# Performance work log

Hardware: AMD Instinct MI355X
Metric: run time of the kernel (lower is better)

Reference implementation:

```python
import jax, jax.numpy as jnp
import numpy as np

EPS = 1e-5

def _rms(x, w):
    v = jnp.mean(jnp.square(x.astype(jnp.float32)), axis=-1, keepdims=True)
    return (x * jax.lax.rsqrt(v + EPS)) * w

def _rope(x, f):
    # x: [B,S,H,hd]; f: [S,1,hd//2,2,2]
    x_ = x.astype(jnp.float32).reshape(*x.shape[:-1], -1, 1, 2)
    out = f[..., 0] * x_[..., 0] + f[..., 1] * x_[..., 1]  # [B,S,H,hd//2,2]
    return out.reshape(x.shape).astype(x.dtype)

def setup_inputs() -> dict:
    key = jax.random.key(0)
    ks = jax.random.split(key, 32)
    B, L, D = 2, 2048, 1024
    ns, enc = 2, 128
    H, hd = 16, 64
    S = enc + L // ns  # 1152 joint seq per stage
    std = 0.02
    w = lambda k, shp: (jax.random.normal(k, shp, jnp.float32) * std)
    inp = {}
    inp['hidden_states'] = jax.random.normal(ks[0], (B, L, D), jnp.float32)
    inp['encoder_hidden_states'] = jax.random.normal(ks[1], (B * ns, enc, D), jnp.float32)
    inp['attention_mask'] = jnp.zeros((ns, B, 1, S, S), jnp.float32)
    inp['image_rotary_emb'] = jax.random.normal(ks[2], (ns, S, 1, hd // 2, 2, 2), jnp.float32)
    names = ['Wq', 'Wk', 'Wv', 'Waq', 'Wak', 'Wav']
    for i, n in enumerate(names):
        inp[n] = w(ks[3 + i], (D, D))
        inp['b' + n[1:]] = jnp.zeros((D,), jnp.float32)
    inp['Wo'] = w(ks[9], (D, D)); inp['bo'] = jnp.zeros((D,), jnp.float32)
    inp['Wao'] = w(ks[10], (D, D)); inp['bao'] = jnp.zeros((D,), jnp.float32)
    for n in ['gq', 'gk', 'gaq', 'gak']:
        inp[n] = jnp.ones((hd,), jnp.float32)
    inp['hidden_length'] = jnp.array([L // ns] * ns, jnp.int32)
    return inp

def reference(hidden_states, encoder_hidden_states, attention_mask, image_rotary_emb,
              Wq, bq, Wk, bk, Wv, bv, Waq, baq, Wak, bak, Wav, bav,
              Wo, bo, Wao, bao, gq, gk, gaq, gak, hidden_length):
    lengths = [int(v) for v in np.asarray(hidden_length)]
    ns = len(lengths)
    B = hidden_states.shape[0]
    enc = encoder_hidden_states.shape[1]
    hd = gq.shape[0]
    H = Wq.shape[0] // hd
    scale = hd ** -0.5
    lin = lambda x, W, b: jnp.einsum('bsd,od->bso', x, W) + b
    proj = lambda x, W, b: lin(x, W, b).reshape(x.shape[0], -1, H, hd)
    q = _rms(proj(hidden_states, Wq, bq), gq)
    k = _rms(proj(hidden_states, Wk, bk), gk)
    v = proj(hidden_states, Wv, bv)
    eq = _rms(proj(encoder_hidden_states, Waq, baq), gaq)
    ek = _rms(proj(encoder_hidden_states, Wak, bak), gak)
    ev = proj(encoder_hidden_states, Wav, bav)
    outs_h, outs_e = [], []
    i_sum = 0
    for i_p, length in enumerate(lengths):
        cq = jnp.concatenate([eq[i_p::ns], q[:, i_sum:i_sum + length]], axis=1)
        ck = jnp.concatenate([ek[i_p::ns], k[:, i_sum:i_sum + length]], axis=1)
        cv = jnp.concatenate([ev[i_p::ns], v[:, i_sum:i_sum + length]], axis=1)
        f = image_rotary_emb[i_p]
        cq = _rope(cq, f)
        ck = _rope(ck, f)
        s = jnp.einsum('bqhd,bkhd->bhqk', cq, ck) * scale + attention_mask[i_p]
        a = jax.nn.softmax(s, axis=-1)
        o = jnp.einsum('bhqk,bkhd->bqhd', a, cv).reshape(B, -1, H * hd)
        outs_e.append(o[:, :enc])
        outs_h.append(o[:, enc:])
        i_sum += length
    enc_out = jnp.stack(outs_e, axis=1).reshape(B * ns, enc, H * hd)
    hid = jnp.concatenate(outs_h, axis=1)
    hid = lin(hid, Wo, bo)
    enc_out = lin(enc_out, Wao, bao)
    return (hid, enc_out)
```

## Files before the change

kernel.cpp:

```cpp
#include <hip/hip_runtime.h>
#include <stdint.h>


typedef unsigned short u16;
typedef unsigned int u32;
typedef short bf16x8 __attribute__((ext_vector_type(8)));
typedef short bf16x4 __attribute__((ext_vector_type(4)));
typedef float f32x4 __attribute__((ext_vector_type(4)));

__device__ __forceinline__ u16 f2bf(float f) {
  union { float f; u32 i; } v; v.f = f;
  u32 u = v.i;
  return (u16)((u + 0x7FFFu + ((u >> 16) & 1u)) >> 16);
}
__device__ __forceinline__ u32 pk2(float a, float b) {
  return (u32)f2bf(a) | ((u32)f2bf(b) << 16);
}

#if __has_builtin(__builtin_amdgcn_mfma_f32_16x16x16_bf16)
#define MFMA16(a, b, c) __builtin_amdgcn_mfma_f32_16x16x16_bf16(a, b, c, 0, 0, 0)
#elif __has_builtin(__builtin_amdgcn_mfma_f32_16x16x16bf16_1k)
#define MFMA16(a, b, c) __builtin_amdgcn_mfma_f32_16x16x16bf16_1k(a, b, c, 0, 0, 0)
#else
__device__ __forceinline__ f32x4 mfma16_asm(bf16x4 a, bf16x4 b, f32x4 c) {
  asm volatile("v_mfma_f32_16x16x16_bf16 %0, %1, %2, %0" : "+v"(c) : "v"(a), "v"(b));
  return c;
}
#define MFMA16(a, b, c) mfma16_asm(a, b, c)
#endif

#define GLD16(g, l)                                                        \
  __builtin_amdgcn_global_load_lds(                                        \
      (const __attribute__((address_space(1))) void*)(uintptr_t)(g),       \
      (__attribute__((address_space(3))) void*)(uintptr_t)(l), 16, 0, 0)

#define WS_QJ 0u
#define WS_KJ 4718592u
#define WS_VT 9437184u
#define WS_OJ 14155776u
#define WS_HS 18874368u
#define WS_EHS 23068672u
#define WS_W0 23592960u

struct ConvArgs {
  const float* src[10];
  u32 dst_off[10];
  u32 blk_prefix[11];
};

__global__ __launch_bounds__(256) void conv_f32_bf16(ConvArgs a, u16* __restrict__ ws) {
  const int b = blockIdx.x;
  int t = 0;
#pragma unroll
  for (int i = 0; i < 9; ++i) t += (b >= (int)a.blk_prefix[i + 1]) ? 1 : 0;
  const int chunk = b - (int)a.blk_prefix[t];
  const int base = chunk * 2048 + threadIdx.x * 8;
  const float4* s = (const float4*)(a.src[t] + base);
  const float4 v0 = s[0];
  const float4 v1 = s[1];
  uint4 o;
  o.x = pk2(v0.x, v0.y); o.y = pk2(v0.z, v0.w);
  o.z = pk2(v1.x, v1.y); o.w = pk2(v1.z, v1.w);
  *(uint4*)(ws + a.dst_off[t] + base) = o;
}

__global__ __launch_bounds__(256) void proj_qkv(
    u16* __restrict__ ws,
    const float* __restrict__ bq, const float* __restrict__ bk, const float* __restrict__ bv,
    const float* __restrict__ baq, const float* __restrict__ bak, const float* __restrict__ bav,
    const float* __restrict__ gq, const float* __restrict__ gk,
    const float* __restrict__ gaq, const float* __restrict__ gak,
    const float* __restrict__ rot) {
  __shared__ __align__(16) char lds[32768];
  const int tid = threadIdx.x;
  const int lane = tid & 63;
  const int w = tid >> 6;
  const int wm = w >> 1, wn = w & 1;
  const int quad = lane >> 4;
  const int l15 = lane & 15;

  const int bx = blockIdx.x;
  const int by = blockIdx.y;
  const int wsel = by >> 3;
  const int nb = by & 7;
  const bool is_enc = (bx >= 32);

  const u16* Asrc = is_enc ? (ws + WS_EHS + (size_t)(bx - 32) * 131072)
                           : (ws + WS_HS + (size_t)bx * 131072);
  const u16* Wsrc = ws + WS_W0 + (size_t)(wsel + (is_enc ? 3 : 0)) * 1048576 +
                    (size_t)nb * 131072;
  const float* bsel;
  const float* gsel = gq;
  if (wsel == 0) { bsel = is_enc ? baq : bq; gsel = is_enc ? gaq : gq; }
  else if (wsel == 1) { bsel = is_enc ? bak : bk; gsel = is_enc ? gak : gk; }
  else { bsel = is_enc ? bav : bv; }

  f32x4 acc[4][4] = {};

  for (int kb = 0; kb < 16; ++kb) {
    __syncthreads();
#pragma unroll
    for (int j = 0; j < 4; ++j) {
      const int sidx = j * 256 + w * 64 + lane;
      const int r = sidx >> 3;
      const int kc = (sidx & 7) ^ (r & 7);
      GLD16(Asrc + (size_t)r * 1024 + kb * 64 + kc * 8, lds + j * 4096 + w * 1024);
      GLD16(Wsrc + (size_t)r * 1024 + kb * 64 + kc * 8, lds + 16384 + j * 4096 + w * 1024);
    }
    __syncthreads();
#pragma unroll
    for (int ks = 0; ks < 2; ++ks) {
      bf16x8 af[4], bw[4];
      const int c = ks * 4 + quad;
#pragma unroll
      for (int t = 0; t < 4; ++t) {
        const int ra = wm * 64 + t * 16 + l15;
        af[t] = *(const bf16x8*)(lds + ra * 128 + ((c ^ (ra & 7)) << 4));
        const int rb = wn * 64 + t * 16 + l15;
        bw[t] = *(const bf16x8*)(lds + 16384 + rb * 128 + ((c ^ (rb & 7)) << 4));
      }
#pragma unroll
      for (int rt = 0; rt < 4; ++rt)
#pragma unroll
        for (int ct = 0; ct < 4; ++ct)
          acc[rt][ct] = __builtin_amdgcn_mfma_f32_16x16x32_bf16(af[rt], bw[ct], acc[rt][ct], 0, 0, 0);
    }
  }

  const int n0 = nb * 128 + wn * 64;
  float biasv[4], gv[4];
#pragma unroll
  for (int ct = 0; ct < 4; ++ct) {
    biasv[ct] = bsel[n0 + ct * 16 + l15];
    gv[ct] = (wsel < 2) ? gsel[ct * 16 + l15] * (wsel == 0 ? 0.125f : 1.0f) : 0.f;
  }

  if (wsel == 2) {
    u16* vt = ws + WS_VT;
#pragma unroll
    for (int rt = 0; rt < 4; ++rt) {
      const int m0 = bx * 128 + wm * 64 + rt * 16 + quad * 4;
      int sb, spos0;
      if (is_enc) {
        const int mp = m0 - 4096;
        const int eb = mp >> 7;
        sb = ((eb & 1) << 1) + (eb >> 1);
        spos0 = mp & 127;
      } else {
        const int b = m0 >> 11;
        const int ip = (m0 >> 10) & 1;
        sb = ip * 2 + b;
        spos0 = 128 + (m0 & 1023);
      }
#pragma unroll
      for (int ct = 0; ct < 4; ++ct) {
        const int d = n0 + ct * 16 + l15;
        uint2 pk;
        pk.x = pk2(acc[rt][ct][0] + biasv[ct], acc[rt][ct][1] + biasv[ct]);
        pk.y = pk2(acc[rt][ct][2] + biasv[ct], acc[rt][ct][3] + biasv[ct]);
        *(uint2*)(vt + (size_t)sb * 1179648 + (size_t)d * 1152 + spos0) = pk;
      }
    }
  } else {
    u16* dst = ws + (wsel == 0 ? WS_QJ : WS_KJ);
#pragma unroll
    for (int rt = 0; rt < 4; ++rt) {
#pragma unroll
      for (int rg = 0; rg < 4; ++rg) {
        const int m = bx * 128 + wm * 64 + rt * 16 + quad * 4 + rg;
        int sb, spos;
        if (is_enc) {
          const int mp = m - 4096;
          const int eb = mp >> 7;
          sb = ((eb & 1) << 1) + (eb >> 1);
          spos = mp & 127;
        } else {
          const int b = m >> 11;
          const int ip = (m >> 10) & 1;
          sb = ip * 2 + b;
          spos = 128 + (m & 1023);
        }
        float vals[4];
#pragma unroll
        for (int ct = 0; ct < 4; ++ct) vals[ct] = acc[rt][ct][rg] + biasv[ct];
        float ssq = vals[0] * vals[0] + vals[1] * vals[1] + vals[2] * vals[2] + vals[3] * vals[3];
        ssq += __shfl_xor(ssq, 1);
        ssq += __shfl_xor(ssq, 2);
        ssq += __shfl_xor(ssq, 4);
        ssq += __shfl_xor(ssq, 8);
        const float sc = rsqrtf(ssq * 0.015625f + 1e-5f);
        const int ip = sb >> 1;
        const float* rf = rot + (size_t)(ip * 1152 + spos) * 128;
#pragma unroll
        for (int ct = 0; ct < 4; ++ct) {
          const float v = vals[ct] * sc * gv[ct];
          const float o = __shfl_xor(v, 1);
          const int d = ct * 16 + l15;
          const float f0 = rf[(d >> 1) * 4 + (d & 1) * 2];
          const float f1 = rf[(d >> 1) * 4 + (d & 1) * 2 + 1];
          vals[ct] = (d & 1) ? (f0 * o + f1 * v) : (f0 * v + f1 * o);
        }
        u16* drow = dst + ((size_t)sb * 1152 + spos) * 1024 + n0;
#pragma unroll
        for (int ct = 0; ct < 4; ++ct) drow[ct * 16 + l15] = f2bf(vals[ct]);
      }
    }
  }
}

__global__ __launch_bounds__(256) void attn(u16* __restrict__ ws) {
  __shared__ __align__(16) char lds[40960];
  const int tid = threadIdx.x;
  const int lane = tid & 63;
  const int w = tid >> 6;
  const int quad = lane >> 4;
  const int l15 = lane & 15;
  const int qb = blockIdx.x;
  const int h = blockIdx.y;
  const int sb = blockIdx.z;

  const u16* Qsrc = ws + WS_QJ + (size_t)sb * 1179648 + h * 64;
  const u16* Ksrc = ws + WS_KJ + (size_t)sb * 1179648 + h * 64;
  const u16* Vsrc = ws + WS_VT + (size_t)sb * 1179648 + (size_t)(h * 64) * 1152;

  char* Qs = lds;
  char* Ks = lds + 8192;
  char* Vt = lds + 24576;

#pragma unroll
  for (int j = 0; j < 2; ++j) {
    const int sidx = j * 256 + w * 64 + lane;
    const int r = sidx >> 3;
    const int kc = (sidx & 7) ^ (r & 7);
    GLD16(Qsrc + (size_t)(qb * 64 + r) * 1024 + kc * 8, Qs + j * 4096 + w * 1024);
  }

  f32x4 oacc[4] = {};
  float m2row = -1e30f, lrow = 0.f;
  const int rqw = w * 16 + l15;
  const float LOG2E = 1.4426950408889634f;

  for (int nc = 0; nc < 9; ++nc) {
    __syncthreads();
#pragma unroll
    for (int j = 0; j < 4; ++j) {
      const int sidx = j * 256 + w * 64 + lane;
      const int r = sidx >> 3;
      const int kc = (sidx & 7) ^ (r & 7);
      GLD16(Ksrc + (size_t)(nc * 128 + r) * 1024 + kc * 8, Ks + j * 4096 + w * 1024);
    }
#pragma unroll
    for (int j = 0; j < 4; ++j) {
      const int sidx = j * 256 + w * 64 + lane;
      const int r = sidx >> 4;
      const int kc = (sidx & 15) ^ (r & 15);
      GLD16(Vsrc + (size_t)r * 1152 + nc * 128 + kc * 8, Vt + j * 4096 + w * 1024);
    }
    __syncthreads();

    f32x4 sacc[8] = {};
#pragma unroll
    for (int ks = 0; ks < 2; ++ks) {
      const int c = ks * 4 + quad;
      const bf16x8 bq = *(const bf16x8*)(Qs + rqw * 128 + ((c ^ (rqw & 7)) << 4));
#pragma unroll
      for (int ct = 0; ct < 8; ++ct) {
        const int rk = ct * 16 + l15;
        const bf16x8 ak = *(const bf16x8*)(Ks + rk * 128 + ((c ^ (rk & 7)) << 4));
        sacc[ct] = __builtin_amdgcn_mfma_f32_16x16x32_bf16(ak, bq, sacc[ct], 0, 0, 0);
      }
    }

    float mx = -1e30f;
#pragma unroll
    for (int ct = 0; ct < 8; ++ct) {
#pragma unroll
      for (int rg = 0; rg < 4; ++rg) {
        sacc[ct][rg] *= LOG2E;
        mx = fmaxf(mx, sacc[ct][rg]);
      }
    }
    mx = fmaxf(mx, __shfl_xor(mx, 16));
    mx = fmaxf(mx, __shfl_xor(mx, 32));
    const float m2new = fmaxf(m2row, mx);
    const float alpha = exp2f(m2row - m2new);
    m2row = m2new;
    float sum = 0.f;
#pragma unroll
    for (int ct = 0; ct < 8; ++ct) {
#pragma unroll
      for (int rg = 0; rg < 4; ++rg) {
        const float p = exp2f(sacc[ct][rg] - m2new);
        sacc[ct][rg] = p;
        sum += p;
      }
    }
    sum += __shfl_xor(sum, 16);
    sum += __shfl_xor(sum, 32);
    lrow = lrow * alpha + sum;

    float alphar[4];
#pragma unroll
    for (int rg = 0; rg < 4; ++rg) alphar[rg] = __shfl(alpha, quad * 4 + rg);
#pragma unroll
    for (int dt = 0; dt < 4; ++dt)
#pragma unroll
      for (int rg = 0; rg < 4; ++rg) oacc[dt][rg] *= alphar[rg];

#pragma unroll
    for (int ct = 0; ct < 8; ++ct) {
      uint2 ap;
      ap.x = pk2(sacc[ct][0], sacc[ct][1]);
      ap.y = pk2(sacc[ct][2], sacc[ct][3]);
      const bf16x4 a4 = *(const bf16x4*)&ap;
      const int gchunk = ct * 2 + (quad >> 1);
      const int sub = (quad & 1) * 8;
#pragma unroll
      for (int dt = 0; dt < 4; ++dt) {
        const int row = dt * 16 + l15;
        const bf16x4 b4 =
            *(const bf16x4*)(Vt + row * 256 + ((gchunk ^ (row & 15)) << 4) + sub);
        oacc[dt] = MFMA16(a4, b4, oacc[dt]);
      }
    }
  }

  const float inv = 1.0f / lrow;
  float invr[4];
#pragma unroll
  for (int rg = 0; rg < 4; ++rg) invr[rg] = __shfl(inv, quad * 4 + rg);
#pragma unroll
  for (int rg = 0; rg < 4; ++rg) {
    const int q = qb * 64 + w * 16 + quad * 4 + rg;
    u16* orow = ws + WS_OJ + ((size_t)sb * 1152 + q) * 1024 + h * 64;
#pragma unroll
    for (int dt = 0; dt < 4; ++dt) orow[dt * 16 + l15] = f2bf(oacc[dt][rg] * invr[rg]);
  }
}

__global__ __launch_bounds__(256) void proj_out(
    u16* __restrict__ ws,
    const float* __restrict__ bo, const float* __restrict__ bao,
    float* __restrict__ out) {
  __shared__ __align__(16) char lds[24576];
  const int tid = threadIdx.x;
  const int lane = tid & 63;
  const int w = tid >> 6;
  const int wm = w >> 1, wn = w & 1;
  const int quad = lane >> 4;
  const int l15 = lane & 15;

  const int bx = blockIdx.x;
  const int nb = blockIdx.y;
  const bool is_enc = (bx >= 64);
  const u16* Oj = ws + WS_OJ;
  const u16* Wsrc = ws + WS_W0 + (size_t)(is_enc ? 7 : 6) * 1048576 + (size_t)nb * 131072;
  const float* bsel = is_enc ? bao : bo;
  float* dstb = is_enc ? (out + 4194304) : out;

  f32x4 acc[2][4] = {};

  for (int kb = 0; kb < 16; ++kb) {
    __syncthreads();
#pragma unroll
    for (int j = 0; j < 2; ++j) {
      const int sidx = j * 256 + w * 64 + lane;
      const int r = sidx >> 3;
      const int kc = (sidx & 7) ^ (r & 7);
      const int m = bx * 64 + r;
      size_t srow;
      if (is_enc) {
        const int mp = m - 4096;
        const int eb = mp >> 7;
        srow = (size_t)((((eb & 1) << 1) + (eb >> 1)) * 1152 + (mp & 127));
      } else {
        const int b = m >> 11;
        const int ip = (m >> 10) & 1;
        srow = (size_t)((ip * 2 + b) * 1152 + 128 + (m & 1023));
      }
      GLD16(Oj + srow * 1024 + kb * 64 + kc * 8, lds + j * 4096 + w * 1024);
    }
#pragma unroll
    for (int j = 0; j < 4; ++j) {
      const int sidx = j * 256 + w * 64 + lane;
      const int r = sidx >> 3;
      const int kc = (sidx & 7) ^ (r & 7);
      GLD16(Wsrc + (size_t)r * 1024 + kb * 64 + kc * 8, lds + 8192 + j * 4096 + w * 1024);
    }
    __syncthreads();
#pragma unroll
    for (int ks = 0; ks < 2; ++ks) {
      bf16x8 af[2], bw[4];
      const int c = ks * 4 + quad;
#pragma unroll
      for (int t = 0; t < 2; ++t) {
        const int ra = wm * 32 + t * 16 + l15;
        af[t] = *(const bf16x8*)(lds + ra * 128 + ((c ^ (ra & 7)) << 4));
      }
#pragma unroll
      for (int ct = 0; ct < 4; ++ct) {
        const int rb = wn * 64 + ct * 16 + l15;
        bw[ct] = *(const bf16x8*)(lds + 8192 + rb * 128 + ((c ^ (rb & 7)) << 4));
      }
#pragma unroll
      for (int rt = 0; rt < 2; ++rt)
#pragma unroll
        for (int ct = 0; ct < 4; ++ct)
          acc[rt][ct] = __builtin_amdgcn_mfma_f32_16x16x32_bf16(af[rt], bw[ct], acc[rt][ct], 0, 0, 0);
    }
  }

  const int n0 = nb * 128 + wn * 64;
  float biasv[4];
#pragma unroll
  for (int ct = 0; ct < 4; ++ct) biasv[ct] = bsel[n0 + ct * 16 + l15];

#pragma unroll
  for (int rt = 0; rt < 2; ++rt) {
#pragma unroll
    for (int rg = 0; rg < 4; ++rg) {
      const int m = bx * 64 + wm * 32 + rt * 16 + quad * 4 + rg;
      const int mout = is_enc ? (m - 4096) : m;
      float* drow = dstb + (size_t)mout * 1024 + n0;
#pragma unroll
      for (int ct = 0; ct < 4; ++ct) drow[ct * 16 + l15] = acc[rt][ct][rg] + biasv[ct];
    }
  }
}

extern "C" void kernel_launch(void* const* d_in, const int* in_sizes, int n_in,
                              void* d_out, int out_size, void* d_ws, size_t ws_size,
                              hipStream_t stream) {
  const float* hs = (const float*)d_in[0];
  const float* ehs = (const float*)d_in[1];
  const float* rot = (const float*)d_in[3];
  const float* Wq = (const float*)d_in[4];   const float* bq = (const float*)d_in[5];
  const float* Wk = (const float*)d_in[6];   const float* bk = (const float*)d_in[7];
  const float* Wv = (const float*)d_in[8];   const float* bv = (const float*)d_in[9];
  const float* Waq = (const float*)d_in[10]; const float* baq = (const float*)d_in[11];
  const float* Wak = (const float*)d_in[12]; const float* bak = (const float*)d_in[13];
  const float* Wav = (const float*)d_in[14]; const float* bav = (const float*)d_in[15];
  const float* Wo = (const float*)d_in[16];  const float* bo = (const float*)d_in[17];
  const float* Wao = (const float*)d_in[18]; const float* bao = (const float*)d_in[19];
  const float* gq = (const float*)d_in[20];  const float* gk = (const float*)d_in[21];
  const float* gaq = (const float*)d_in[22]; const float* gak = (const float*)d_in[23];

  u16* ws = (u16*)d_ws;

  ConvArgs ca;
  ca.src[0] = hs;  ca.dst_off[0] = WS_HS;
  ca.src[1] = ehs; ca.dst_off[1] = WS_EHS;
  const float* Wlist[8] = {Wq, Wk, Wv, Waq, Wak, Wav, Wo, Wao};
  for (int i = 0; i < 8; ++i) { ca.src[2 + i] = Wlist[i]; ca.dst_off[2 + i] = WS_W0 + i * 1048576u; }
  u32 pre = 0;
  const u32 blks[10] = {2048, 256, 512, 512, 512, 512, 512, 512, 512, 512};
  for (int i = 0; i < 10; ++i) { ca.blk_prefix[i] = pre; pre += blks[i]; }
  ca.blk_prefix[10] = pre;

  conv_f32_bf16<<<pre, 256, 0, stream>>>(ca, ws);
  proj_qkv<<<dim3(36, 24), 256, 0, stream>>>(ws, bq, bk, bv, baq, bak, bav,
                                             gq, gk, gaq, gak, rot);
  attn<<<dim3(18, 16, 4), 256, 0, stream>>>(ws);
  proj_out<<<dim3(72, 8), 256, 0, stream>>>(ws, bo, bao, (float*)d_out);
}
```

Before: 277.2 us.

## Double-buffer LDS tiles in QKV and output projection GEMMs

Both projection GEMM kernels now stage K-tiles into two alternating LDS buffers. The loads for tile kb+1 are issued right after the barrier and before the MFMA work on tile kb, so global-to-LDS latency overlaps with compute instead of being exposed every iteration. In exchange, per-block shared memory doubles (64KB and 48KB), which can reduce the number of resident blocks per CU.

```diff
diff --git a/kernel.cpp b/kernel.cpp
--- a/kernel.cpp
+++ b/kernel.cpp
@@ -71,7 +71,7 @@
     const float* __restrict__ gq, const float* __restrict__ gk,
     const float* __restrict__ gaq, const float* __restrict__ gak,
     const float* __restrict__ rot) {
-  __shared__ __align__(16) char lds[32768];
+  __shared__ __align__(16) char lds[65536];
   const int tid = threadIdx.x;
   const int lane = tid & 63;
   const int w = tid >> 6;
@@ -97,17 +97,23 @@
 
   f32x4 acc[4][4] = {};
 
-  for (int kb = 0; kb < 16; ++kb) {
-    __syncthreads();
+  auto stage = [&](int kb, char* base) {
 #pragma unroll
     for (int j = 0; j < 4; ++j) {
       const int sidx = j * 256 + w * 64 + lane;
       const int r = sidx >> 3;
       const int kc = (sidx & 7) ^ (r & 7);
-      GLD16(Asrc + (size_t)r * 1024 + kb * 64 + kc * 8, lds + j * 4096 + w * 1024);
-      GLD16(Wsrc + (size_t)r * 1024 + kb * 64 + kc * 8, lds + 16384 + j * 4096 + w * 1024);
-    }
+      GLD16(Asrc + (size_t)r * 1024 + kb * 64 + kc * 8, base + j * 4096 + w * 1024);
+      GLD16(Wsrc + (size_t)r * 1024 + kb * 64 + kc * 8, base + 16384 + j * 4096 + w * 1024);
+    }
+  };
+
+  stage(0, lds);
+  for (int kb = 0; kb < 16; ++kb) {
+    char* cur = lds + (kb & 1) * 32768;
+    char* nxt = lds + ((kb + 1) & 1) * 32768;
     __syncthreads();
+    if (kb < 15) stage(kb + 1, nxt);
 #pragma unroll
     for (int ks = 0; ks < 2; ++ks) {
       bf16x8 af[4], bw[4];
@@ -115,9 +121,9 @@
 #pragma unroll
       for (int t = 0; t < 4; ++t) {
         const int ra = wm * 64 + t * 16 + l15;
-        af[t] = *(const bf16x8*)(lds + ra * 128 + ((c ^ (ra & 7)) << 4));
+        af[t] = *(const bf16x8*)(cur + ra * 128 + ((c ^ (ra & 7)) << 4));
         const int rb = wn * 64 + t * 16 + l15;
-        bw[t] = *(const bf16x8*)(lds + 16384 + rb * 128 + ((c ^ (rb & 7)) << 4));
+        bw[t] = *(const bf16x8*)(cur + 16384 + rb * 128 + ((c ^ (rb & 7)) << 4));
       }
 #pragma unroll
       for (int rt = 0; rt < 4; ++rt)
@@ -342,7 +348,7 @@
     u16* __restrict__ ws,
     const float* __restrict__ bo, const float* __restrict__ bao,
     float* __restrict__ out) {
-  __shared__ __align__(16) char lds[24576];
+  __shared__ __align__(16) char lds[49152];
   const int tid = threadIdx.x;
   const int lane = tid & 63;
   const int w = tid >> 6;
@@ -360,8 +366,7 @@
 
   f32x4 acc[2][4] = {};
 
-  for (int kb = 0; kb < 16; ++kb) {
-    __syncthreads();
+  auto stage = [&](int kb, char* base) {
 #pragma unroll
     for (int j = 0; j < 2; ++j) {
       const int sidx = j * 256 + w * 64 + lane;
@@ -378,16 +383,23 @@
         const int ip = (m >> 10) & 1;
         srow = (size_t)((ip * 2 + b) * 1152 + 128 + (m & 1023));
       }
-      GLD16(Oj + srow * 1024 + kb * 64 + kc * 8, lds + j * 4096 + w * 1024);
+      GLD16(Oj + srow * 1024 + kb * 64 + kc * 8, base + j * 4096 + w * 1024);
     }
 #pragma unroll
     for (int j = 0; j < 4; ++j) {
       const int sidx = j * 256 + w * 64 + lane;
       const int r = sidx >> 3;
       const int kc = (sidx & 7) ^ (r & 7);
-      GLD16(Wsrc + (size_t)r * 1024 + kb * 64 + kc * 8, lds + 8192 + j * 4096 + w * 1024);
-    }
+      GLD16(Wsrc + (size_t)r * 1024 + kb * 64 + kc * 8, base + 8192 + j * 4096 + w * 1024);
+    }
+  };
+
+  stage(0, lds);
+  for (int kb = 0; kb < 16; ++kb) {
+    char* cur = lds + (kb & 1) * 24576;
+    char* nxt = lds + ((kb + 1) & 1) * 24576;
     __syncthreads();
+    if (kb < 15) stage(kb + 1, nxt);
 #pragma unroll
     for (int ks = 0; ks < 2; ++ks) {
       bf16x8 af[2], bw[4];
@@ -395,12 +407,12 @@
 #pragma unroll
       for (int t = 0; t < 2; ++t) {
         const int ra = wm * 32 + t * 16 + l15;
-        af[t] = *(const bf16x8*)(lds + ra * 128 + ((c ^ (ra & 7)) << 4));
+        af[t] = *(const bf16x8*)(cur + ra * 128 + ((c ^ (ra & 7)) << 4));
       }
 #pragma unroll
       for (int ct = 0; ct < 4; ++ct) {
         const int rb = wn * 64 + ct * 16 + l15;
-        bw[ct] = *(const bf16x8*)(lds + 8192 + rb * 128 + ((c ^ (rb & 7)) << 4));
+        bw[ct] = *(const bf16x8*)(cur + 8192 + rb * 128 + ((c ^ (rb & 7)) << 4));
       }
 #pragma unroll
       for (int rt = 0; rt < 2; ++rt)
```

Measured after the change: 274.7 us. Within noise of the previous version (-0.9%).
